# Optimization experiments

Hardware: AMD Instinct MI355X
Metric: run time of the kernel (lower is better)

The kernel has to match this reference:

```python
import jax, jax.numpy as jnp
import numpy as np

NEG_INF = -jnp.inf


def conv2d(x, w, b, stride, pad):
    # x: [B,C,H,W], w: [O,I,kh,kw]
    y = jax.lax.conv_general_dilated(
        x, w, window_strides=(stride, stride),
        padding=[(pad, pad), (pad, pad)],
        dimension_numbers=('NCHW', 'OIHW', 'NCHW'))
    return y + b[None, :, None, None]


def maxpool3s2(x):
    return jax.lax.reduce_window(x, -jnp.inf, jax.lax.max,
                                 (1, 1, 3, 3), (1, 1, 2, 2), 'VALID')


def setup_inputs() -> dict:
    key = jax.random.key(0)
    ks = jax.random.split(key, 20)
    s = 0.02
    B, C, H, W = 64, 3, 224, 224
    D, HID, OUT, E = 9216, 288, 1000, 8   # feature_dim, hidden_dim, output_dim, n_experts
    GH = 72                               # gate hidden = hidden_dim // 4
    inp = {
        'x':   jax.random.normal(ks[0], (B, C, H, W), jnp.float32),
        'c1w': s * jax.random.normal(ks[1], (64, 3, 11, 11), jnp.float32),
        'c1b': jnp.zeros((64,), jnp.float32),
        'c2w': s * jax.random.normal(ks[2], (192, 64, 5, 5), jnp.float32),
        'c2b': jnp.zeros((192,), jnp.float32),
        'c3w': s * jax.random.normal(ks[3], (384, 192, 3, 3), jnp.float32),
        'c3b': jnp.zeros((384,), jnp.float32),
        'c4w': s * jax.random.normal(ks[4], (256, 384, 3, 3), jnp.float32),
        'c4b': jnp.zeros((256,), jnp.float32),
        'c5w': s * jax.random.normal(ks[5], (256, 256, 3, 3), jnp.float32),
        'c5b': jnp.zeros((256,), jnp.float32),
        'gw1': s * jax.random.normal(ks[6], (D, GH), jnp.float32),
        'gb1': jnp.zeros((GH,), jnp.float32),
        'gw2': s * jax.random.normal(ks[7], (GH, E), jnp.float32),
        'gb2': jnp.zeros((E,), jnp.float32),
        'ew1': s * jax.random.normal(ks[8], (E, D, HID), jnp.float32),
        'eb1': jnp.zeros((E, HID), jnp.float32),
        'ew2': s * jax.random.normal(ks[9], (E, HID, HID // 2), jnp.float32),
        'eb2': jnp.zeros((E, HID // 2), jnp.float32),
        'ew3': s * jax.random.normal(ks[10], (E, HID // 2, OUT), jnp.float32),
        'eb3': jnp.zeros((E, OUT), jnp.float32),
    }
    return inp


def reference(x, c1w, c1b, c2w, c2b, c3w, c3b, c4w, c4b, c5w, c5b,
              gw1, gb1, gw2, gb2, ew1, eb1, ew2, eb2, ew3, eb3):
    # ---- AlexNet-style feature extractor (224 branch) ----
    h = jax.nn.relu(conv2d(x, c1w, c1b, 4, 2))   # [B,64,55,55]
    h = maxpool3s2(h)                             # [B,64,27,27]
    h = jax.nn.relu(conv2d(h, c2w, c2b, 1, 2))   # [B,192,27,27]
    h = maxpool3s2(h)                             # [B,192,13,13]
    h = jax.nn.relu(conv2d(h, c3w, c3b, 1, 1))   # [B,384,13,13]
    h = jax.nn.relu(conv2d(h, c4w, c4b, 1, 1))   # [B,256,13,13]
    h = jax.nn.relu(conv2d(h, c5w, c5b, 1, 1))   # [B,256,13,13]
    h = maxpool3s2(h)                             # [B,256,6,6]
    # AdaptiveAvgPool2d((6,6)) on a 6x6 input is the identity.
    feat = h.reshape(h.shape[0], -1)              # [B,9216]

    # ---- Gate: top-2 routing (eval mode: no noise, no dropout) ----
    g = jax.nn.relu(feat @ gw1 + gb1)             # [B,72]
    logits = g @ gw2 + gb2                        # [B,8]
    topv, topi = jax.lax.top_k(logits, 2)         # [B,2]
    topw = jax.nn.softmax(topv, axis=-1)          # softmax over top-2 only
    B = logits.shape[0]
    gates = jnp.zeros_like(logits).at[jnp.arange(B)[:, None], topi].set(topw)  # [B,8]

    # ---- Dense per-expert 3-layer MLP over full batch (as in source) ----
    h1 = jax.nn.relu(jnp.einsum('bd,edh->ebh', feat, ew1) + eb1[:, None, :])   # [E,B,288]
    h2 = jax.nn.relu(jnp.einsum('ebh,ehk->ebk', h1, ew2) + eb2[:, None, :])    # [E,B,144]
    eo = jnp.einsum('ebk,eko->ebo', h2, ew3) + eb3[:, None, :]                 # [E,B,1000]
    # Weighted combine; gates are zero for non-top-2 experts, matching the
    # masked accumulation loop in the torch forward.
    out = jnp.einsum('ebo,be->bo', eo, gates)     # [B,1000]
    return out
```

## Files before the change

kernel.cpp:

```cpp
#include <hip/hip_runtime.h>
#include <math.h>

#define TPB 256

typedef short s16x8 __attribute__((ext_vector_type(8)));
typedef short s16x4 __attribute__((ext_vector_type(4)));
typedef float f32x4 __attribute__((ext_vector_type(4)));

__device__ inline void bsplit(float x, short& h, short& l){
  union { float f; unsigned u; } a, hf, rf;
  a.f = x;
  unsigned hu = (a.u + 0x7FFFu + ((a.u >> 16) & 1u)) >> 16;
  h = (short)hu;
  hf.u = hu << 16;
  rf.f = x - hf.f;
  l = (short)((rf.u + 0x7FFFu + ((rf.u >> 16) & 1u)) >> 16);
}
__device__ inline float b2f(short s){
  union { unsigned u; float f; } x;
  x.u = ((unsigned)(unsigned short)s) << 16;
  return x.f;
}

__global__ __launch_bounds__(TPB) void wsplit_k(
    const float* __restrict__ w, short* __restrict__ wh, short* __restrict__ wl,
    int C, int O, int ntap, int total)
{
  int idx = blockIdx.x*TPB + threadIdx.x;
  if (idx >= total) return;
  int c   = idx % C;
  int t2  = idx / C;
  int oc  = t2 % O;
  int tap = t2 / O;
  float x = w[((size_t)oc*C + c)*ntap + tap];
  short h, l; bsplit(x, h, l);
  int tile = oc >> 4, ln = oc & 15;
  int S    = ntap*(C >> 5);
  int sl   = tap*(C >> 5) + (c >> 5);
  int lg   = (c >> 3) & 3, j = c & 7;
  size_t dst = (((size_t)tile*S + sl)*64 + lg*16 + ln)*8 + j;
  wh[dst] = h; wl[dst] = l;
}

__global__ __launch_bounds__(TPB) void wsplit1_k(
    const float* __restrict__ w, short* __restrict__ wh, short* __restrict__ wl)
{
  int idx = blockIdx.x*TPB + threadIdx.x;
  if (idx >= 64*576) return;
  int k  = idx % 576;
  int oc = idx / 576;
  int g  = k >> 4, kw = k & 15;
  int c  = g / 12, kh = g % 12;
  float x = 0.f;
  if (kh < 11 && kw < 11)
    x = w[((size_t)oc*3 + c)*121 + kh*11 + kw];
  short h, l; bsplit(x, h, l);
  int m = oc >> 4, ln = oc & 15;
  int s = k >> 5, r = k & 31;
  int lg = r >> 3, j = r & 7;
  size_t dst = (((size_t)m*18 + s)*64 + lg*16 + ln)*8 + j;
  wh[dst] = h; wl[dst] = l;
}

__global__ __launch_bounds__(TPB) void wtrans_k(
    const float* __restrict__ w, float* __restrict__ wT, int K, int O)
{
  int idx = blockIdx.x*TPB + threadIdx.x;
  if (idx >= K*O) return;
  int oc = idx % O;
  int k  = idx / O;
  wT[idx] = w[(size_t)oc*K + k];
}

#define C1W 240
#define CV1_PL 33
__global__ __launch_bounds__(256, 4) void conv1m_k(
    const float* __restrict__ in, const short* __restrict__ whi,
    const short* __restrict__ wlo, const float* __restrict__ bias,
    short* __restrict__ yh, short* __restrict__ yl)
{
  __shared__ __align__(16) short lds[2][CV1_PL*C1W + 84];
  const int tid = threadIdx.x;
  const int oh = blockIdx.x % 55;
  const int b  = blockIdx.x / 55;
  const int nt = tid >> 6;
  const int ln = tid & 15;
  const int lg = (tid & 63) >> 4;
  const int lane = tid & 63;
  const int ow = nt*16 + ln;

  const float* ip = in + (size_t)b*3*224*224;
  for (int i = tid; i < CV1_PL*59; i += 256){
    int plane = i / 59;
    int p     = i % 59;
    int c = plane / 11, kh = plane % 11;
    int ih = oh*4 - 2 + kh;
    int col0 = p*4;
    const float* rowp = (ih >= 0 && ih < 224) ? ip + (size_t)c*50176 + (size_t)ih*224 : nullptr;
    short h[4], l[4];
    #pragma unroll
    for (int j=0;j<4;++j){
      int iw = col0 + j - 2;
      float v = (rowp && iw >= 0 && iw < 224) ? rowp[iw] : 0.f;
      bsplit(v, h[j], l[j]);
    }
    s16x4 hv = {h[0],h[1],h[2],h[3]}, lv = {l[0],l[1],l[2],l[3]};
    *reinterpret_cast<s16x4*>(&lds[0][plane*C1W + col0]) = hv;
    *reinterpret_cast<s16x4*>(&lds[1][plane*C1W + col0]) = lv;
  }
  __syncthreads();

  f32x4 acc[4];
  #pragma unroll
  for (int m=0;m<4;++m){
    const float4 bv = *reinterpret_cast<const float4*>(bias + m*16 + lg*4);
    acc[m] = (f32x4){bv.x, bv.y, bv.z, bv.w};
  }

  s16x8 ah[4], al[4], ahn[4], aln[4];
  #pragma unroll
  for (int m=0;m<4;++m){
    size_t ao = (((size_t)m*18 + 0)*64 + lane)*8;
    ah[m] = *reinterpret_cast<const s16x8*>(whi + ao);
    al[m] = *reinterpret_cast<const s16x8*>(wlo + ao);
  }

  #pragma unroll 1
  for (int s=0; s<18; ++s){
    if (s < 17){
      #pragma unroll
      for (int m=0;m<4;++m){
        size_t ao = (((size_t)m*18 + s + 1)*64 + lane)*8;
        ahn[m] = *reinterpret_cast<const s16x8*>(whi + ao);
        aln[m] = *reinterpret_cast<const s16x8*>(wlo + ao);
      }
    }
    int g  = 2*s + (lg >> 1);
    int c  = g / 12, kh = g % 12;
    int plane = c*11 + (kh < 11 ? kh : 10);
    int base  = plane*C1W + ow*4 + (lg & 1)*8;
    s16x4 h0 = *reinterpret_cast<const s16x4*>(&lds[0][base]);
    s16x4 h1 = *reinterpret_cast<const s16x4*>(&lds[0][base+4]);
    s16x4 l0 = *reinterpret_cast<const s16x4*>(&lds[1][base]);
    s16x4 l1 = *reinterpret_cast<const s16x4*>(&lds[1][base+4]);
    s16x8 bh = __builtin_shufflevector(h0, h1, 0,1,2,3,4,5,6,7);
    s16x8 bl = __builtin_shufflevector(l0, l1, 0,1,2,3,4,5,6,7);
    #pragma unroll
    for (int m=0;m<4;++m){
      acc[m] = __builtin_amdgcn_mfma_f32_16x16x32_bf16(al[m], bh, acc[m], 0,0,0);
      acc[m] = __builtin_amdgcn_mfma_f32_16x16x32_bf16(ah[m], bl, acc[m], 0,0,0);
      acc[m] = __builtin_amdgcn_mfma_f32_16x16x32_bf16(ah[m], bh, acc[m], 0,0,0);
    }
    #pragma unroll
    for (int m=0;m<4;++m){ ah[m] = ahn[m]; al[m] = aln[m]; }
  }

  if (ow < 55){
    size_t base = ((size_t)b*3025 + (size_t)oh*55 + ow)*64;
    #pragma unroll
    for (int m=0;m<4;++m){
      short h[4], l[4];
      #pragma unroll
      for (int r=0;r<4;++r) bsplit(fmaxf(acc[m][r], 0.f), h[r], l[r]);
      s16x4 hv = {h[0],h[1],h[2],h[3]}, lv = {l[0],l[1],l[2],l[3]};
      *reinterpret_cast<s16x4*>(yh + base + m*16 + lg*4) = hv;
      *reinterpret_cast<s16x4*>(yl + base + m*16 + lg*4) = lv;
    }
  }
}

__global__ __launch_bounds__(TPB) void pool1_k(
    const short* __restrict__ xh, const short* __restrict__ xl,
    short* __restrict__ yh, short* __restrict__ yl)
{
  int i = blockIdx.x*TPB + threadIdx.x;
  if (i >= 64*729*64) return;
  int c = i & 63;
  int t = i >> 6;
  int sp = t % 729;
  int b = t / 729;
  int r = sp/27, cc = sp%27;
  const short* ph = xh + (size_t)b*3025*64 + c;
  const short* pl = xl + (size_t)b*3025*64 + c;
  float m = -INFINITY;
  #pragma unroll
  for (int di=0;di<3;++di)
    #pragma unroll
    for (int dj=0;dj<3;++dj){
      size_t s = (size_t)((2*r+di)*55 + 2*cc+dj)*64;
      m = fmaxf(m, b2f(ph[s]) + b2f(pl[s]));
    }
  short h, l; bsplit(m, h, l);
  yh[i] = h; yl[i] = l;
}

__global__ __launch_bounds__(256, 3) void conv2m_k(
    const short* __restrict__ xh, const short* __restrict__ xl,
    const short* __restrict__ whi, const short* __restrict__ wlo,
    const float* __restrict__ bias, short* __restrict__ yh, short* __restrict__ yl)
{
  __shared__ __align__(16) short lds[2][217*40];
  const int tid = threadIdx.x;
  const int rg  = blockIdx.x;
  const int b   = blockIdx.y;
  const int wid = tid >> 6;
  const int ln  = tid & 15;
  const int lg  = (tid & 63) >> 4;
  const int lane = tid & 63;
  const int oc0 = wid*48;
  const int r0  = rg*3;

  int sb[6], nn[6];
  #pragma unroll
  for (int t=0;t<6;++t){
    int n = t*16 + ln;
    nn[t] = n;
    int ohl = n / 27, ow = n % 27;
    sb[t] = (n < 81) ? (ohl*31 + ow) : 0;
  }

  f32x4 acc[3][6];
  #pragma unroll
  for (int m=0;m<3;++m){
    const float4 bv = *reinterpret_cast<const float4*>(bias + oc0 + m*16 + lg*4);
    #pragma unroll
    for (int t=0;t<6;++t) acc[m][t] = (f32x4){bv.x, bv.y, bv.z, bv.w};
  }

  #pragma unroll 1
  for (int c0=0; c0<64; c0+=32){
    __syncthreads();
    for (int i = tid; i < 217*4; i += 256){
      int sp = i >> 2, v = i & 3;
      int pr = sp/31, pc = sp%31;
      int ih = r0 - 2 + pr, iw = pc - 2;
      s16x8 hv = {0,0,0,0,0,0,0,0}, lv = {0,0,0,0,0,0,0,0};
      if (ih >= 0 && ih < 27 && iw >= 0 && iw < 27){
        size_t o = ((size_t)b*729 + ih*27 + iw)*64 + c0 + v*8;
        hv = *reinterpret_cast<const s16x8*>(xh + o);
        lv = *reinterpret_cast<const s16x8*>(xl + o);
      }
      *reinterpret_cast<s16x8*>(&lds[0][sp*40 + v*8]) = hv;
      *reinterpret_cast<s16x8*>(&lds[1][sp*40 + v*8]) = lv;
    }
    __syncthreads();

    const size_t tstr = 50*512;
    const size_t abase = ((size_t)(wid*3)*50 + (c0 >> 5))*512 + (size_t)lane*8;
    s16x8 ah0 = *reinterpret_cast<const s16x8*>(whi + abase);
    s16x8 ah1 = *reinterpret_cast<const s16x8*>(whi + abase + tstr);
    s16x8 ah2 = *reinterpret_cast<const s16x8*>(whi + abase + 2*tstr);
    s16x8 al0 = *reinterpret_cast<const s16x8*>(wlo + abase);
    s16x8 al1 = *reinterpret_cast<const s16x8*>(wlo + abase + tstr);
    s16x8 al2 = *reinterpret_cast<const s16x8*>(wlo + abase + 2*tstr);

    #pragma unroll 1
    for (int tap=0; tap<25; ++tap){
      s16x8 nh0=ah0, nh1=ah1, nh2=ah2, nl0=al0, nl1=al1, nl2=al2;
      if (tap < 24){
        size_t ao = abase + (size_t)(tap+1)*2*512;
        nh0 = *reinterpret_cast<const s16x8*>(whi + ao);
        nh1 = *reinterpret_cast<const s16x8*>(whi + ao + tstr);
        nh2 = *reinterpret_cast<const s16x8*>(whi + ao + 2*tstr);
        nl0 = *reinterpret_cast<const s16x8*>(wlo + ao);
        nl1 = *reinterpret_cast<const s16x8*>(wlo + ao + tstr);
        nl2 = *reinterpret_cast<const s16x8*>(wlo + ao + 2*tstr);
      }
      const int toff = (tap/5)*31 + (tap%5);
      #pragma unroll
      for (int t=0;t<6;++t){
        int off = (sb[t] + toff)*40 + lg*8;
        s16x8 bh = *reinterpret_cast<const s16x8*>(&lds[0][off]);
        s16x8 bl = *reinterpret_cast<const s16x8*>(&lds[1][off]);
        acc[0][t] = __builtin_amdgcn_mfma_f32_16x16x32_bf16(al0, bh, acc[0][t], 0,0,0);
        acc[0][t] = __builtin_amdgcn_mfma_f32_16x16x32_bf16(ah0, bl, acc[0][t], 0,0,0);
        acc[0][t] = __builtin_amdgcn_mfma_f32_16x16x32_bf16(ah0, bh, acc[0][t], 0,0,0);
        acc[1][t] = __builtin_amdgcn_mfma_f32_16x16x32_bf16(al1, bh, acc[1][t], 0,0,0);
        acc[1][t] = __builtin_amdgcn_mfma_f32_16x16x32_bf16(ah1, bl, acc[1][t], 0,0,0);
        acc[1][t] = __builtin_amdgcn_mfma_f32_16x16x32_bf16(ah1, bh, acc[1][t], 0,0,0);
        acc[2][t] = __builtin_amdgcn_mfma_f32_16x16x32_bf16(al2, bh, acc[2][t], 0,0,0);
        acc[2][t] = __builtin_amdgcn_mfma_f32_16x16x32_bf16(ah2, bl, acc[2][t], 0,0,0);
        acc[2][t] = __builtin_amdgcn_mfma_f32_16x16x32_bf16(ah2, bh, acc[2][t], 0,0,0);
      }
      ah0=nh0; ah1=nh1; ah2=nh2; al0=nl0; al1=nl1; al2=nl2;
    }
  }

  #pragma unroll
  for (int m=0;m<3;++m)
    #pragma unroll
    for (int t=0;t<6;++t){
      if (nn[t] < 81){
        int gsp = r0*27 + nn[t];
        size_t base = ((size_t)b*729 + gsp)*192 + oc0 + m*16 + lg*4;
        short h[4], l[4];
        #pragma unroll
        for (int r=0;r<4;++r) bsplit(fmaxf(acc[m][t][r], 0.f), h[r], l[r]);
        s16x4 hv = {h[0],h[1],h[2],h[3]}, lv = {l[0],l[1],l[2],l[3]};
        *reinterpret_cast<s16x4*>(yh + base) = hv;
        *reinterpret_cast<s16x4*>(yl + base) = lv;
      }
    }
}

__global__ __launch_bounds__(TPB) void pool2_k(
    const short* __restrict__ xh, const short* __restrict__ xl,
    short* __restrict__ yh, short* __restrict__ yl)
{
  int i = blockIdx.x*TPB + threadIdx.x;
  if (i >= 64*169*192) return;
  int c = i % 192;
  int t = i / 192;
  int sp = t % 169;
  int b = t / 169;
  int r = sp/13, cc = sp%13;
  const short* ph = xh + (size_t)b*729*192 + c;
  const short* pl = xl + (size_t)b*729*192 + c;
  float m = -INFINITY;
  #pragma unroll
  for (int di=0;di<3;++di)
    #pragma unroll
    for (int dj=0;dj<3;++dj){
      size_t s = (size_t)((2*r+di)*27 + 2*cc+dj)*192;
      m = fmaxf(m, b2f(ph[s]) + b2f(pl[s]));
    }
  short h, l; bsplit(m, h, l);
  yh[i] = h; yl[i] = l;
}

template<int C,int O>
__global__ __launch_bounds__(256, 3) void conv3m_k(
    const short* __restrict__ xh, const short* __restrict__ xl,
    const short* __restrict__ whi, const short* __restrict__ wlo,
    const float* __restrict__ bias, short* __restrict__ yh, short* __restrict__ yl)
{
  __shared__ __align__(16) short lds[2][225*40];
  const int tid = threadIdx.x;
  const int b   = blockIdx.y;
  const int wid = tid >> 6;
  const int ln  = tid & 15;
  const int lg  = (tid & 63) >> 4;
  const int lane = tid & 63;
  const int tileIdx = blockIdx.x*2 + (wid & 1);
  const int oc0 = tileIdx*16;
  const int ng  = wid >> 1;
  const int tbase  = ng ? 6 : 0;
  const int ntiles = ng ? 5 : 6;
  const int S3 = 9*(C/32);

  int sb[6], nn[6];
  #pragma unroll
  for (int t=0;t<6;++t){
    int n = (tbase + t)*16 + ln;
    nn[t] = n;
    int oh = n / 13, ow = n % 13;
    sb[t] = (n < 169) ? (oh*15 + ow) : 0;
  }

  f32x4 acc[6];
  const float4 bv = *reinterpret_cast<const float4*>(bias + oc0 + lg*4);
  #pragma unroll
  for (int t=0;t<6;++t) acc[t] = (f32x4){bv.x, bv.y, bv.z, bv.w};

  #pragma unroll 1
  for (int c0=0; c0<C; c0+=32){
    __syncthreads();
    for (int i = tid; i < 225*4; i += 256){
      int sp = i >> 2, v = i & 3;
      int r = sp/15, cc = sp%15;
      s16x8 hv = {0,0,0,0,0,0,0,0}, lv = {0,0,0,0,0,0,0,0};
      if (r >= 1 && r <= 13 && cc >= 1 && cc <= 13){
        size_t o = ((size_t)b*169 + (r-1)*13 + (cc-1))*C + c0 + v*8;
        hv = *reinterpret_cast<const s16x8*>(xh + o);
        lv = *reinterpret_cast<const s16x8*>(xl + o);
      }
      *reinterpret_cast<s16x8*>(&lds[0][sp*40 + v*8]) = hv;
      *reinterpret_cast<s16x8*>(&lds[1][sp*40 + v*8]) = lv;
    }
    __syncthreads();

    const size_t tb = (size_t)tileIdx*S3 + (c0 >> 5);
    s16x8 ah = *reinterpret_cast<const s16x8*>(whi + (tb*64 + lane)*8);
    s16x8 al = *reinterpret_cast<const s16x8*>(wlo + (tb*64 + lane)*8);
    #pragma unroll 1
    for (int tap=0; tap<9; ++tap){
      s16x8 ahn = ah, aln = al;
      if (tap < 8){
        size_t ao = ((tb + (size_t)(tap+1)*(C/32))*64 + lane)*8;
        ahn = *reinterpret_cast<const s16x8*>(whi + ao);
        aln = *reinterpret_cast<const s16x8*>(wlo + ao);
      }
      const int toff = (tap/3)*15 + (tap%3);
      #pragma unroll
      for (int t=0;t<6;++t){
        if (t < ntiles){
          int off = (sb[t] + toff)*40 + lg*8;
          s16x8 bh = *reinterpret_cast<const s16x8*>(&lds[0][off]);
          s16x8 bl = *reinterpret_cast<const s16x8*>(&lds[1][off]);
          acc[t] = __builtin_amdgcn_mfma_f32_16x16x32_bf16(al, bh, acc[t], 0,0,0);
          acc[t] = __builtin_amdgcn_mfma_f32_16x16x32_bf16(ah, bl, acc[t], 0,0,0);
          acc[t] = __builtin_amdgcn_mfma_f32_16x16x32_bf16(ah, bh, acc[t], 0,0,0);
        }
      }
      ah = ahn; al = aln;
    }
  }

  #pragma unroll
  for (int t=0;t<6;++t){
    if (t < ntiles && nn[t] < 169){
      size_t base = ((size_t)b*169 + nn[t])*O + oc0 + lg*4;
      short h[4], l[4];
      #pragma unroll
      for (int r=0;r<4;++r) bsplit(fmaxf(acc[t][r], 0.f), h[r], l[r]);
      s16x4 hv = {h[0],h[1],h[2],h[3]}, lv = {l[0],l[1],l[2],l[3]};
      *reinterpret_cast<s16x4*>(yh + base) = hv;
      *reinterpret_cast<s16x4*>(yl + base) = lv;
    }
  }
}

__global__ __launch_bounds__(TPB) void pool3_k(
    const short* __restrict__ xh, const short* __restrict__ xl,
    float* __restrict__ feat)
{
  int i = blockIdx.x*TPB + threadIdx.x;
  if (i >= 64*9216) return;
  int d = i % 9216;
  int b = i / 9216;
  int c = d / 36;
  int sp = d % 36;
  int r = sp/6, cc = sp%6;
  const short* ph = xh + (size_t)b*169*256 + c;
  const short* pl = xl + (size_t)b*169*256 + c;
  float m = -INFINITY;
  #pragma unroll
  for (int di=0;di<3;++di)
    #pragma unroll
    for (int dj=0;dj<3;++dj){
      size_t s = (size_t)((2*r+di)*13 + 2*cc+dj)*256;
      m = fmaxf(m, b2f(ph[s]) + b2f(pl[s]));
    }
  feat[i] = m;
}

__global__ __launch_bounds__(TPB) void featsplit_k(
    const float* __restrict__ feat, short* __restrict__ fbh, short* __restrict__ fbl)
{
  int idx = blockIdx.x*TPB + threadIdx.x;
  if (idx >= 589824) return;
  int j = idx & 7;
  int lane = (idx >> 3) & 63;
  int nt = (idx >> 9) & 3;
  int s = idx >> 11;
  int b = nt*16 + (lane & 15);
  int d = s*32 + (lane >> 4)*8 + j;
  short h, l; bsplit(feat[(size_t)b*9216 + d], h, l);
  fbh[idx] = h; fbl[idx] = l;
}

__global__ __launch_bounds__(256) void gate1_k(
    const float* __restrict__ feat, const float* __restrict__ gw1T,
    const float* __restrict__ gb1, float* __restrict__ g)
{
  const int b    = blockIdx.x;
  const int h    = blockIdx.y*4 + (threadIdx.x >> 6);
  const int lane = threadIdx.x & 63;
  const float* f = feat + (size_t)b*9216;
  const float* w = gw1T + (size_t)h*9216;
  float s = 0.f;
  #pragma unroll
  for (int it=0; it<36; ++it){
    int d = it*256 + lane*4;
    float4 fv = *reinterpret_cast<const float4*>(f + d);
    float4 wv = *reinterpret_cast<const float4*>(w + d);
    s = fmaf(fv.x, wv.x, s);
    s = fmaf(fv.y, wv.y, s);
    s = fmaf(fv.z, wv.z, s);
    s = fmaf(fv.w, wv.w, s);
  }
  #pragma unroll
  for (int off=32; off; off>>=1) s += __shfl_down(s, off, 64);
  if (lane == 0) g[(size_t)b*72 + h] = fmaxf(s + gb1[h], 0.f);
}

__global__ __launch_bounds__(128) void gate2_k(
    const float* __restrict__ g, const float* __restrict__ gw2,
    const float* __restrict__ gb2, float* __restrict__ gates)
{
  const int b = blockIdx.x;
  const int tid = threadIdx.x;
  __shared__ float gs[72];
  __shared__ float logits[8];
  if (tid < 72) gs[tid] = g[(size_t)b*72 + tid];
  __syncthreads();
  if (tid < 8) {
    float acc = gb2[tid];
    for (int j=0;j<72;++j)
      acc = fmaf(gs[j], gw2[(size_t)j*8 + tid], acc);
    logits[tid] = acc;
  }
  __syncthreads();
  if (tid == 0) {
    int i1 = 0; float v1 = logits[0];
    for (int e=1;e<8;++e) if (logits[e] > v1) { v1 = logits[e]; i1 = e; }
    int i2 = -1; float v2 = -INFINITY;
    for (int e=0;e<8;++e) { if (e==i1) continue; if (logits[e] > v2) { v2 = logits[e]; i2 = e; } }
    float z  = expf(v2 - v1);
    float w1 = 1.f / (1.f + z);
    float w2 = z   / (1.f + z);
    float* gr = gates + (size_t)b*8;
    for (int e=0;e<8;++e) gr[e] = 0.f;
    gr[i1] = w1;
    gr[i2] = w2;
  }
}

__global__ __launch_bounds__(256, 4) void eh1m_k(
    const float* __restrict__ ew1, const short* __restrict__ fbh,
    const short* __restrict__ fbl, float* __restrict__ part)
{
  __shared__ __align__(16) short wh_l[32*88];
  __shared__ __align__(16) short wl_l[32*88];
  const int m2 = blockIdx.x;
  const int e  = blockIdx.y;
  const int ks = blockIdx.z;
  const int tid = threadIdx.x;
  const int nt = tid >> 6;
  const int ln = tid & 15;
  const int lg = (tid & 63) >> 4;
  const int lane = tid & 63;

  f32x4 acc[2] = {(f32x4){0.f,0.f,0.f,0.f},(f32x4){0.f,0.f,0.f,0.f}};

  const float* wsrc = ew1 + (size_t)e*9216*288 + (size_t)m2*32;
  const int d0 = ks*576;

  #pragma unroll 1
  for (int st=0; st<9; ++st){
    __syncthreads();
    {
      int drow = tid >> 2;
      int h0 = (tid & 3)*8;
      const float* src = wsrc + (size_t)(d0 + st*64 + drow)*288 + h0;
      float4 v0 = *reinterpret_cast<const float4*>(src);
      float4 v1 = *reinterpret_cast<const float4*>(src+4);
      float vv[8] = {v0.x,v0.y,v0.z,v0.w,v1.x,v1.y,v1.z,v1.w};
      #pragma unroll
      for (int k=0;k<8;++k){
        short h, l; bsplit(vv[k], h, l);
        wh_l[(h0+k)*88 + drow] = h;
        wl_l[(h0+k)*88 + drow] = l;
      }
    }
    __syncthreads();
    int sg = (d0 + st*64) >> 5;
    #pragma unroll
    for (int sl=0; sl<2; ++sl){
      size_t bo = ((size_t)(sg+sl)*4 + nt)*512 + (size_t)lane*8;
      s16x8 bh = *reinterpret_cast<const s16x8*>(fbh + bo);
      s16x8 bl = *reinterpret_cast<const s16x8*>(fbl + bo);
      #pragma unroll
      for (int m=0;m<2;++m){
        int ao = (m*16 + ln)*88 + sl*32 + lg*8;
        s16x8 ah = *reinterpret_cast<const s16x8*>(&wh_l[ao]);
        s16x8 al = *reinterpret_cast<const s16x8*>(&wl_l[ao]);
        acc[m] = __builtin_amdgcn_mfma_f32_16x16x32_bf16(al, bh, acc[m], 0,0,0);
        acc[m] = __builtin_amdgcn_mfma_f32_16x16x32_bf16(ah, bl, acc[m], 0,0,0);
        acc[m] = __builtin_amdgcn_mfma_f32_16x16x32_bf16(ah, bh, acc[m], 0,0,0);
      }
    }
  }
  #pragma unroll
  for (int m=0;m<2;++m){
    int h = m2*32 + m*16 + lg*4;
    int b = nt*16 + ln;
    float* pp = part + ((size_t)(ks*8+e)*288 + h)*64 + b;
    #pragma unroll
    for (int r=0;r<4;++r)
      pp[(size_t)r*64] = acc[m][r];
  }
}

__global__ __launch_bounds__(TPB) void eh1_reduce_k(
    const float* __restrict__ part, const float* __restrict__ eb1,
    float* __restrict__ h1)
{
  int idx = blockIdx.x*TPB + threadIdx.x;
  if (idx >= 8*288*64) return;
  int b = idx & 63;
  int h = (idx >> 6) % 288;
  int e = idx / (64*288);
  float a = eb1[(size_t)e*288 + h];
  #pragma unroll
  for (int s=0;s<16;++s)
    a += part[((size_t)(s*8+e)*288 + h)*64 + b];
  h1[((size_t)e*64 + b)*288 + h] = fmaxf(a, 0.f);
}

__global__ __launch_bounds__(TPB) void expert_h2_k(
    const float* __restrict__ h1, const float* __restrict__ ew2,
    const float* __restrict__ eb2, const float* __restrict__ gates,
    float* __restrict__ h2)
{
  int idx = blockIdx.x*TPB + threadIdx.x;
  if (idx >= 8*64*144) return;
  int k = idx % 144;
  int t = idx / 144;
  int b = t % 64;
  int e = t / 64;
  if (gates[(size_t)b*8 + e] == 0.f) return;
  float acc = eb2[(size_t)e*144 + k];
  const float* h = h1 + ((size_t)e*64 + b)*288;
  const float* w = ew2 + (size_t)e*288*144 + k;
  for (int d=0; d<288; ++d)
    acc = fmaf(h[d], w[(size_t)d*144], acc);
  h2[idx] = fmaxf(acc, 0.f);
}

__global__ __launch_bounds__(TPB) void expert_out_k(
    const float* __restrict__ h2, const float* __restrict__ ew3,
    const float* __restrict__ eb3, const float* __restrict__ gates,
    float* __restrict__ out)
{
  int idx = blockIdx.x*TPB + threadIdx.x;
  if (idx >= 64*1000) return;
  int o = idx % 1000;
  int b = idx / 1000;
  float acc = 0.f;
  const float* gr = gates + (size_t)b*8;
  for (int e=0;e<8;++e){
    float ge = gr[e];
    if (ge == 0.f) continue;
    float a = eb3[(size_t)e*1000 + o];
    const float* h = h2 + ((size_t)e*64 + b)*144;
    const float* w = ew3 + (size_t)e*144*1000 + o;
    for (int k=0;k<144;++k)
      a = fmaf(h[k], w[(size_t)k*1000], a);
    acc = fmaf(ge, a, acc);
  }
  out[idx] = acc;
}

static inline int nblk(long long n){ return (int)((n + TPB - 1) / TPB); }

extern "C" void kernel_launch(void* const* d_in, const int* in_sizes, int n_in,
                              void* d_out, int out_size, void* d_ws, size_t ws_size,
                              hipStream_t stream)
{
  const float* x   = (const float*)d_in[0];
  const float* c1w = (const float*)d_in[1];  const float* c1b = (const float*)d_in[2];
  const float* c2w = (const float*)d_in[3];  const float* c2b = (const float*)d_in[4];
  const float* c3w = (const float*)d_in[5];  const float* c3b = (const float*)d_in[6];
  const float* c4w = (const float*)d_in[7];  const float* c4b = (const float*)d_in[8];
  const float* c5w = (const float*)d_in[9];  const float* c5b = (const float*)d_in[10];
  const float* gw1 = (const float*)d_in[11]; const float* gb1 = (const float*)d_in[12];
  const float* gw2 = (const float*)d_in[13]; const float* gb2 = (const float*)d_in[14];
  const float* ew1 = (const float*)d_in[15]; const float* eb1 = (const float*)d_in[16];
  const float* ew2 = (const float*)d_in[17]; const float* eb2 = (const float*)d_in[18];
  const float* ew3 = (const float*)d_in[19]; const float* eb3 = (const float*)d_in[20];
  float* out = (float*)d_out;

  float* W = (float*)d_ws;
  short* X1H = (short*)W;
  short* X1L = X1H + 12390400;
  short* X3H = (short*)W;
  short* X3L = X3H + 8957952;
  short* X5H = (short*)W;
  short* X5L = X5H + 4153344;
  short* X7H = (short*)W;
  short* X7L = X7H + 2768896;
  float* feat  = W + 5000000;
  short* FBH   = (short*)(W + 5600000);
  short* FBL   = (short*)(W + 5900000);
  float* part  = W + 6300000;
  short* WH2 = (short*)(W +  9000000);
  short* WL2 = WH2 + 307200;
  short* WH3 = (short*)(W +  9320000);
  short* WL3 = WH3 + 663552;
  short* WH4 = (short*)(W + 10000000);
  short* WL4 = WH4 + 884736;
  short* WH5 = (short*)(W + 10900000);
  short* WL5 = WH5 + 589824;
  float* GT1 = W + 11500000;
  short* X2H = (short*)(W + 12390400);
  short* X2L = X2H + 2985984;
  short* X4H = (short*)(W + 12390400);
  short* X4L = X4H + 2076672;
  short* X6H = (short*)(W + 12390400);
  short* X6L = X6H + 2768896;
  float* gates = W + 14000000;
  float* h1    = gates + 512;
  float* h2    = h1 + 147456;
  float* gbuf  = h2 + 73728;
  short* WH1 = (short*)(W + 15400000);
  short* WL1 = WH1 + 36864;
  (void)ws_size; (void)in_sizes; (void)n_in; (void)out_size;

  wsplit1_k<<<nblk(64LL*576), TPB, 0, stream>>>(c1w, WH1, WL1);
  conv1m_k<<<55*64, 256, 0, stream>>>(x, WH1, WL1, c1b, X1H, X1L);
  pool1_k<<<nblk(64LL*729*64), TPB, 0, stream>>>(X1H, X1L, X2H, X2L);
  wsplit_k<<<nblk(25LL*192*64),  TPB, 0, stream>>>(c2w, WH2, WL2,  64, 192, 25, 25*192*64);
  wsplit_k<<<nblk(9LL*384*192),  TPB, 0, stream>>>(c3w, WH3, WL3, 192, 384,  9, 9*384*192);
  wsplit_k<<<nblk(9LL*256*384),  TPB, 0, stream>>>(c4w, WH4, WL4, 384, 256,  9, 9*256*384);
  wsplit_k<<<nblk(9LL*256*256),  TPB, 0, stream>>>(c5w, WH5, WL5, 256, 256,  9, 9*256*256);
  wtrans_k<<<nblk(72LL*9216),    TPB, 0, stream>>>(gw1, GT1, 72, 9216);

  conv2m_k<<<dim3(9,64), 256, 0, stream>>>(X2H, X2L, WH2, WL2, c2b, X3H, X3L);
  pool2_k<<<nblk(64LL*169*192), TPB, 0, stream>>>(X3H, X3L, X4H, X4L);
  conv3m_k<192,384><<<dim3(12,64), 256, 0, stream>>>(X4H, X4L, WH3, WL3, c3b, X5H, X5L);
  conv3m_k<384,256><<<dim3(8,64),  256, 0, stream>>>(X5H, X5L, WH4, WL4, c4b, X6H, X6L);
  conv3m_k<256,256><<<dim3(8,64),  256, 0, stream>>>(X6H, X6L, WH5, WL5, c5b, X7H, X7L);
  pool3_k<<<nblk(64LL*9216), TPB, 0, stream>>>(X7H, X7L, feat);

  gate1_k<<<dim3(64,18), 256, 0, stream>>>(feat, GT1, gb1, gbuf);
  gate2_k<<<64, 128, 0, stream>>>(gbuf, gw2, gb2, gates);

  featsplit_k<<<nblk(589824LL), TPB, 0, stream>>>(feat, FBH, FBL);
  eh1m_k<<<dim3(9,8,16), 256, 0, stream>>>(ew1, FBH, FBL, part);
  eh1_reduce_k<<<nblk(8LL*288*64), TPB, 0, stream>>>(part, eb1, h1);
  expert_h2_k<<<nblk(8LL*64*144), TPB, 0, stream>>>(h1, ew2, eb2, gates, h2);
  expert_out_k<<<nblk(64LL*1000), TPB, 0, stream>>>(h2, ew3, eb3, gates, out);
}
```

Before: 534.2 us.

## Fuse conv1 with maxpool1, computing three conv rows per block

The conv1 kernel now computes the three conv output rows that feed one pooled row per block, sharing the loaded weight fragments across those rows. It applies ReLU into an LDS buffer and performs the 3x3 stride-2 maxpool in place. The separate pool kernel and the large X1 intermediate round trip through global memory go away. In exchange, LDS use per block grows, occupancy drops (launch bound 2) and the grid shrinks to 27x64 blocks. One conv row is recomputed between adjacent pooled rows.

```diff
diff --git a/kernel.cpp b/kernel.cpp
--- a/kernel.cpp
+++ b/kernel.cpp
@@ -73,16 +73,15 @@
 }
 
 #define C1W 240
-#define CV1_PL 33
-__global__ __launch_bounds__(256, 4) void conv1m_k(
+__global__ __launch_bounds__(256, 2) void conv1p_k(
     const float* __restrict__ in, const short* __restrict__ whi,
     const short* __restrict__ wlo, const float* __restrict__ bias,
     short* __restrict__ yh, short* __restrict__ yl)
 {
-  __shared__ __align__(16) short lds[2][CV1_PL*C1W + 84];
+  __shared__ __align__(16) short lds[2][57*C1W + 84];
   const int tid = threadIdx.x;
-  const int oh = blockIdx.x % 55;
-  const int b  = blockIdx.x / 55;
+  const int r  = blockIdx.x;
+  const int b  = blockIdx.y;
   const int nt = tid >> 6;
   const int ln = tid & 15;
   const int lg = (tid & 63) >> 4;
@@ -90,11 +89,11 @@
   const int ow = nt*16 + ln;
 
   const float* ip = in + (size_t)b*3*224*224;
-  for (int i = tid; i < CV1_PL*59; i += 256){
+  for (int i = tid; i < 57*59; i += 256){
     int plane = i / 59;
     int p     = i % 59;
-    int c = plane / 11, kh = plane % 11;
-    int ih = oh*4 - 2 + kh;
+    int c = plane / 19, ri = plane % 19;
+    int ih = 8*r - 2 + ri;
     int col0 = p*4;
     const float* rowp = (ih >= 0 && ih < 224) ? ip + (size_t)c*50176 + (size_t)ih*224 : nullptr;
     short h[4], l[4];
@@ -110,11 +109,13 @@
   }
   __syncthreads();
 
-  f32x4 acc[4];
+  f32x4 acc[3][4];
   #pragma unroll
   for (int m=0;m<4;++m){
     const float4 bv = *reinterpret_cast<const float4*>(bias + m*16 + lg*4);
-    acc[m] = (f32x4){bv.x, bv.y, bv.z, bv.w};
+    #pragma unroll
+    for (int sub=0;sub<3;++sub)
+      acc[sub][m] = (f32x4){bv.x, bv.y, bv.z, bv.w};
   }
 
   s16x8 ah[4], al[4], ahn[4], aln[4];
@@ -137,61 +138,55 @@
     }
     int g  = 2*s + (lg >> 1);
     int c  = g / 12, kh = g % 12;
-    int plane = c*11 + (kh < 11 ? kh : 10);
-    int base  = plane*C1W + ow*4 + (lg & 1)*8;
-    s16x4 h0 = *reinterpret_cast<const s16x4*>(&lds[0][base]);
-    s16x4 h1 = *reinterpret_cast<const s16x4*>(&lds[0][base+4]);
-    s16x4 l0 = *reinterpret_cast<const s16x4*>(&lds[1][base]);
-    s16x4 l1 = *reinterpret_cast<const s16x4*>(&lds[1][base+4]);
-    s16x8 bh = __builtin_shufflevector(h0, h1, 0,1,2,3,4,5,6,7);
-    s16x8 bl = __builtin_shufflevector(l0, l1, 0,1,2,3,4,5,6,7);
-    #pragma unroll
-    for (int m=0;m<4;++m){
-      acc[m] = __builtin_amdgcn_mfma_f32_16x16x32_bf16(al[m], bh, acc[m], 0,0,0);
-      acc[m] = __builtin_amdgcn_mfma_f32_16x16x32_bf16(ah[m], bl, acc[m], 0,0,0);
-      acc[m] = __builtin_amdgcn_mfma_f32_16x16x32_bf16(ah[m], bh, acc[m], 0,0,0);
+    int khp = (kh < 11) ? kh : 10;
+    #pragma unroll
+    for (int sub=0;sub<3;++sub){
+      int plane = c*19 + 4*sub + khp;
+      int base  = plane*C1W + ow*4 + (lg & 1)*8;
+      s16x4 h0 = *reinterpret_cast<const s16x4*>(&lds[0][base]);
+      s16x4 h1 = *reinterpret_cast<const s16x4*>(&lds[0][base+4]);
+      s16x4 l0 = *reinterpret_cast<const s16x4*>(&lds[1][base]);
+      s16x4 l1 = *reinterpret_cast<const s16x4*>(&lds[1][base+4]);
+      s16x8 bh = __builtin_shufflevector(h0, h1, 0,1,2,3,4,5,6,7);
+      s16x8 bl = __builtin_shufflevector(l0, l1, 0,1,2,3,4,5,6,7);
+      #pragma unroll
+      for (int m=0;m<4;++m){
+        acc[sub][m] = __builtin_amdgcn_mfma_f32_16x16x32_bf16(al[m], bh, acc[sub][m], 0,0,0);
+        acc[sub][m] = __builtin_amdgcn_mfma_f32_16x16x32_bf16(ah[m], bl, acc[sub][m], 0,0,0);
+        acc[sub][m] = __builtin_amdgcn_mfma_f32_16x16x32_bf16(ah[m], bh, acc[sub][m], 0,0,0);
+      }
     }
     #pragma unroll
     for (int m=0;m<4;++m){ ah[m] = ahn[m]; al[m] = aln[m]; }
   }
 
+  __syncthreads();
+  float* convbuf = (float*)&lds[0][0];
   if (ow < 55){
-    size_t base = ((size_t)b*3025 + (size_t)oh*55 + ow)*64;
-    #pragma unroll
-    for (int m=0;m<4;++m){
-      short h[4], l[4];
-      #pragma unroll
-      for (int r=0;r<4;++r) bsplit(fmaxf(acc[m][r], 0.f), h[r], l[r]);
-      s16x4 hv = {h[0],h[1],h[2],h[3]}, lv = {l[0],l[1],l[2],l[3]};
-      *reinterpret_cast<s16x4*>(yh + base + m*16 + lg*4) = hv;
-      *reinterpret_cast<s16x4*>(yl + base + m*16 + lg*4) = lv;
-    }
-  }
-}
-
-__global__ __launch_bounds__(TPB) void pool1_k(
-    const short* __restrict__ xh, const short* __restrict__ xl,
-    short* __restrict__ yh, short* __restrict__ yl)
-{
-  int i = blockIdx.x*TPB + threadIdx.x;
-  if (i >= 64*729*64) return;
-  int c = i & 63;
-  int t = i >> 6;
-  int sp = t % 729;
-  int b = t / 729;
-  int r = sp/27, cc = sp%27;
-  const short* ph = xh + (size_t)b*3025*64 + c;
-  const short* pl = xl + (size_t)b*3025*64 + c;
-  float m = -INFINITY;
-  #pragma unroll
-  for (int di=0;di<3;++di)
-    #pragma unroll
-    for (int dj=0;dj<3;++dj){
-      size_t s = (size_t)((2*r+di)*55 + 2*cc+dj)*64;
-      m = fmaxf(m, b2f(ph[s]) + b2f(pl[s]));
-    }
-  short h, l; bsplit(m, h, l);
-  yh[i] = h; yl[i] = l;
+    #pragma unroll
+    for (int sub=0;sub<3;++sub)
+      #pragma unroll
+      for (int m=0;m<4;++m)
+        #pragma unroll
+        for (int rr=0;rr<4;++rr){
+          int oc = m*16 + lg*4 + rr;
+          convbuf[(sub*64 + oc)*57 + ow] = fmaxf(acc[sub][m][rr], 0.f);
+        }
+  }
+  __syncthreads();
+
+  for (int i = tid; i < 27*64; i += 256){
+    int pw = i >> 6, c = i & 63;
+    float m = -INFINITY;
+    #pragma unroll
+    for (int sub=0;sub<3;++sub)
+      #pragma unroll
+      for (int j=0;j<3;++j)
+        m = fmaxf(m, convbuf[(sub*64 + c)*57 + 2*pw + j]);
+    short h, l; bsplit(m, h, l);
+    size_t o = ((size_t)b*729 + r*27 + pw)*64 + c;
+    yh[o] = h; yl[o] = l;
+  }
 }
 
 __global__ __launch_bounds__(256, 3) void conv2m_k(
@@ -662,8 +657,6 @@
   float* out = (float*)d_out;
 
   float* W = (float*)d_ws;
-  short* X1H = (short*)W;
-  short* X1L = X1H + 12390400;
   short* X3H = (short*)W;
   short* X3L = X3H + 8957952;
   short* X5H = (short*)W;
@@ -698,8 +691,7 @@
   (void)ws_size; (void)in_sizes; (void)n_in; (void)out_size;
 
   wsplit1_k<<<nblk(64LL*576), TPB, 0, stream>>>(c1w, WH1, WL1);
-  conv1m_k<<<55*64, 256, 0, stream>>>(x, WH1, WL1, c1b, X1H, X1L);
-  pool1_k<<<nblk(64LL*729*64), TPB, 0, stream>>>(X1H, X1L, X2H, X2L);
+  conv1p_k<<<dim3(27,64), 256, 0, stream>>>(x, WH1, WL1, c1b, X2H, X2L);
   wsplit_k<<<nblk(25LL*192*64),  TPB, 0, stream>>>(c2w, WH2, WL2,  64, 192, 25, 25*192*64);
   wsplit_k<<<nblk(9LL*384*192),  TPB, 0, stream>>>(c3w, WH3, WL3, 192, 384,  9, 9*384*192);
   wsplit_k<<<nblk(9LL*256*384),  TPB, 0, stream>>>(c4w, WH4, WL4, 384, 256,  9, 9*256*384);
```

After: 513.0 us. -4.0%, faster.
